# Kernel tuning notes

Measured on AMD Instinct MI355X. Metric: run time of the kernel, lower is better.

## Reference

```python
import jax, jax.numpy as jnp
import numpy as np

B, N, E, H = 2, 2048, 1024, 16
D = E // H  # head dim = 64


def layer_norm(x, gamma, beta, eps=1e-5):
    m = jnp.mean(x, axis=-1, keepdims=True)
    v = jnp.mean(jnp.square(x - m), axis=-1, keepdims=True)
    return (x - m) * jax.lax.rsqrt(v + eps) * gamma + beta


def setup_inputs() -> dict:
    key = jax.random.key(0)
    ks = jax.random.split(key, 9)
    w_scale = 1.0 / np.sqrt(E)
    Q = jax.random.normal(ks[0], (B, N, E), jnp.float32)
    K = jax.random.normal(ks[1], (B, N, E), jnp.float32)
    V = jax.random.normal(ks[2], (B, N, E), jnp.float32)
    # causal mask: True = masked (matches torch masked_fill_ semantics)
    mask = jnp.broadcast_to(jnp.triu(jnp.ones((N, N), bool), k=1)[None, None], (B, 1, N, N))
    Wq = jax.random.normal(ks[3], (E, E), jnp.float32) * w_scale
    Wk = jax.random.normal(ks[4], (E, E), jnp.float32) * w_scale
    Wv = jax.random.normal(ks[5], (E, E), jnp.float32) * w_scale
    bq = jax.random.normal(ks[6], (E,), jnp.float32) * 0.02
    bk = jax.random.normal(ks[7], (E,), jnp.float32) * 0.02
    bv = jax.random.normal(ks[8], (E,), jnp.float32) * 0.02
    gamma = jnp.ones((E,), jnp.float32)
    beta = jnp.zeros((E,), jnp.float32)
    return dict(Q=Q, K=K, V=V, mask=mask, Wq=Wq, bq=bq, Wk=Wk, bk=bk,
                Wv=Wv, bv=bv, gamma=gamma, beta=beta)


def reference(Q, K, V, mask, Wq, bq, Wk, bk, Wv, bv, gamma, beta):
    resid = Q  # cloned_Q residual
    # pre-norm (same LayerNorm applied to all three streams)
    q = layer_norm(Q, gamma, beta) @ Wq + bq  # [B,N,E]
    k = layer_norm(K, gamma, beta) @ Wk + bk
    v = layer_norm(V, gamma, beta) @ Wv + bv
    # split heads -> [B,H,N,D]
    q = q.reshape(B, N, H, D).transpose(0, 2, 1, 3)
    k = k.reshape(B, N, H, D).transpose(0, 2, 1, 3)
    v = v.reshape(B, N, H, D).transpose(0, 2, 1, 3)
    # scores [B,H,N,N], scaled by sqrt(head_dim)
    s = jnp.einsum('bhnd,bhmd->bhnm', q, k) * (D ** -0.5)
    s = jnp.where(mask, -jnp.inf, s)
    p = jax.nn.softmax(s, axis=-1)
    o = jnp.einsum('bhnm,bhmd->bhnd', p, v)
    o = o.transpose(0, 2, 1, 3).reshape(B, N, E)
    return o + resid
```

## Files before the change

### kernel.cpp

```cpp
#include <hip/hip_runtime.h>
#include <hip/hip_bf16.h>

#define B_ 2
#define N_ 2048
#define E_ 1024
#define H_ 16
#define D_ 64
#define M_TOT (B_*N_)

typedef __attribute__((ext_vector_type(8))) short bf16x8;
typedef __attribute__((ext_vector_type(4))) float f32x4;

__device__ __forceinline__ unsigned short f2bf(float f) {
    unsigned int u = __float_as_uint(f);
    u += 0x7fff + ((u >> 16) & 1);
    return (unsigned short)(u >> 16);
}

__device__ __forceinline__ void gload16(const void* g, void* l) {
    __builtin_amdgcn_global_load_lds(
        (const __attribute__((address_space(1))) unsigned int*)g,
        (__attribute__((address_space(3))) unsigned int*)l, 16, 0, 0);
}

__global__ __launch_bounds__(256) void ln_kernel(
    const float* __restrict__ Q, const float* __restrict__ K,
    const float* __restrict__ V, const float* __restrict__ gamma,
    const float* __restrict__ beta, unsigned short* __restrict__ Xn)
{
    const int row = blockIdx.x;
    const int s   = blockIdx.y;
    const float* X = (s == 0) ? Q : (s == 1) ? K : V;
    const int tid = threadIdx.x;
    const float4 x = ((const float4*)(X + (size_t)row * E_))[tid];
    float sum = x.x + x.y + x.z + x.w;
    float sq  = x.x*x.x + x.y*x.y + x.z*x.z + x.w*x.w;
    #pragma unroll
    for (int off = 32; off > 0; off >>= 1) {
        sum += __shfl_down(sum, off);
        sq  += __shfl_down(sq,  off);
    }
    __shared__ float red[8];
    const int wid = tid >> 6;
    if ((tid & 63) == 0) { red[wid] = sum; red[4 + wid] = sq; }
    __syncthreads();
    if (tid == 0) {
        float s0 = red[0] + red[1] + red[2] + red[3];
        float q0 = red[4] + red[5] + red[6] + red[7];
        red[0] = s0 * (1.0f / E_);
        red[4] = q0 * (1.0f / E_);
    }
    __syncthreads();
    const float mean = red[0];
    const float var  = red[4] - mean * mean;
    const float inv  = rsqrtf(var + 1e-5f);
    const float4 g = ((const float4*)gamma)[tid];
    const float4 b = ((const float4*)beta)[tid];
    ushort4 o;
    o.x = f2bf((x.x - mean) * inv * g.x + b.x);
    o.y = f2bf((x.y - mean) * inv * g.y + b.y);
    o.z = f2bf((x.z - mean) * inv * g.z + b.z);
    o.w = f2bf((x.w - mean) * inv * g.w + b.w);
    const int bo = 8 * tid;
    const int bs = (bo & ~127) | ((bo & 127) ^ ((row & 7) << 4));
    char* rowp = (char*)(Xn + (size_t)s * M_TOT * E_ + (size_t)row * E_);
    *(ushort4*)(rowp + bs) = o;
}

__global__ __launch_bounds__(256) void wt_kernel(
    const float* __restrict__ Wq, const float* __restrict__ Wk,
    const float* __restrict__ Wv, unsigned short* __restrict__ Wt)
{
    const int s = blockIdx.z;
    const float* W = (s == 0) ? Wq : (s == 1) ? Wk : Wv;
    __shared__ float tile[32][33];
    const int tx = threadIdx.x, ty = threadIdx.y;
    const int n0 = blockIdx.x * 32, k0 = blockIdx.y * 32;
    #pragma unroll
    for (int i = 0; i < 4; i++)
        tile[ty + 8*i][tx] = W[(size_t)(k0 + ty + 8*i) * E_ + n0 + tx];
    __syncthreads();
    unsigned short* dst = Wt + (size_t)s * E_ * E_;
    #pragma unroll
    for (int i = 0; i < 4; i++) {
        const int n = n0 + ty + 8*i;
        const int bo = 2 * (k0 + tx);
        const int bs = (bo & ~127) | ((bo & 127) ^ ((n & 7) << 4));
        *(unsigned short*)((char*)(dst + (size_t)n * E_) + bs) =
            f2bf(tile[tx][ty + 8*i]);
    }
}

__global__ __launch_bounds__(256, 3) void gemm_kernel(
    const unsigned short* __restrict__ Xn, const unsigned short* __restrict__ Wt,
    const float* __restrict__ bq, const float* __restrict__ bk,
    const float* __restrict__ bv, unsigned short* __restrict__ QKVh)
{
    const int bid = blockIdx.x;
    const int wk  = (bid & 7) * 96 + (bid >> 3);
    const int s   = wk >> 8;
    const int rem = wk & 255;
    const int m0  = (rem >> 3) * 128;
    const int n0  = (rem & 7) * 128;
    const float* bias = (s == 0) ? bq : (s == 1) ? bk : bv;
    const unsigned short* A  = Xn + (size_t)s * M_TOT * E_;
    const unsigned short* Bw = Wt + (size_t)s * E_ * E_;
    unsigned short* out = QKVh + (size_t)s * M_TOT * E_;
    const int tid = threadIdx.x;
    const int lane = tid & 63;
    const int w = tid >> 6;
    const int l15 = lane & 15, lhi = lane >> 4;

    __shared__ unsigned short Al[2][128][64];

    const int srow = lane >> 3;
    const int scol = (lane & 7) * 8;
    const int rx = (l15 & 7) << 4;

    const char* bbase = (const char*)Bw + (size_t)(n0 + w*32 + l15) * (E_ * 2);

    f32x4 acc[8][2];
    #pragma unroll
    for (int m = 0; m < 8; m++)
        #pragma unroll
        for (int n = 0; n < 2; n++)
            acc[m][n] = (f32x4){0.f, 0.f, 0.f, 0.f};

    #define STAGEA(b_, kt_) do {                                             \
        const int k0_ = (kt_) * 64;                                          \
        _Pragma("unroll")                                                    \
        for (int ii = 0; ii < 4; ii++) {                                     \
            const int r_ = w*32 + ii*8;                                      \
            gload16(A + (size_t)(m0 + r_ + srow) * E_ + k0_ + scol,          \
                    &Al[b_][r_][0]);                                         \
        }                                                                    \
    } while (0)

    STAGEA(0, 0);
    for (int kt = 0; kt < 16; kt++) {
        const int buf = kt & 1;
        bf16x8 bfr[2][2];
        #pragma unroll
        for (int ks = 0; ks < 2; ks++)
            #pragma unroll
            for (int n = 0; n < 2; n++)
                bfr[ks][n] = *(const bf16x8*)(bbase + (size_t)n * 16 * (E_ * 2)
                               + kt*128 + ((ks*64 + lhi*16) ^ rx));
        __syncthreads();
        if (kt + 1 < 16) STAGEA(buf ^ 1, kt + 1);
        const char* ab = (const char*)Al[buf];
        #pragma unroll
        for (int ks = 0; ks < 2; ks++) {
            #pragma unroll
            for (int m = 0; m < 8; m++) {
                bf16x8 af = *(const bf16x8*)(ab
                        + (m*16 + l15)*128 + ((ks*64 + lhi*16) ^ rx));
                #pragma unroll
                for (int n = 0; n < 2; n++)
                    acc[m][n] = __builtin_amdgcn_mfma_f32_16x16x32_bf16(
                        af, bfr[ks][n], acc[m][n], 0, 0, 0);
            }
        }
    }
    #undef STAGEA

    const float scale = (s == 0) ? 0.18033688011112042f : 1.0f;
    #pragma unroll
    for (int n = 0; n < 2; n++) {
        const int gn = n0 + w*32 + n*16 + l15;
        const float bv_ = bias[gn];
        const int h = gn >> 6, d = gn & 63;
        #pragma unroll
        for (int m = 0; m < 8; m++) {
            const int gmBase = m0 + m*16 + lhi*4;
            if (s == 2) {
                const int bb2 = gmBase >> 11, nseq = gmBase & 2047;
                ushort4 pk;
                pk.x = f2bf(acc[m][n][0] + bv_);
                pk.y = f2bf(acc[m][n][1] + bv_);
                pk.z = f2bf(acc[m][n][2] + bv_);
                pk.w = f2bf(acc[m][n][3] + bv_);
                *(ushort4*)(out + ((size_t)(bb2*H_ + h) * D_ + d) * N_ + nseq)
                    = pk;
            } else {
                #pragma unroll
                for (int j = 0; j < 4; j++) {
                    const int gm = gmBase + j;
                    const int bb2 = gm >> 11, nseq = gm & 2047;
                    out[((size_t)(bb2*H_ + h) * N_ + nseq) * D_ + d] =
                        f2bf((acc[m][n][j] + bv_) * scale);
                }
            }
        }
    }
}

__global__ __launch_bounds__(512, 4) void attn_kernel(
    const unsigned short* __restrict__ QKVh, const float* __restrict__ Qin,
    float* __restrict__ out)
{
    const int bid  = blockIdx.x;
    const int slot = bid >> 5;
    const int bh   = bid & 31;
    const int g    = 31 - slot;
    const int q0   = g * 64;
    const int S    = (g + 2) >> 1;
    const int tid = threadIdx.x;
    const int lane = tid & 63;
    const int w = tid >> 6;
    const int h = w >> 2;
    const int rg = w & 3;
    const int l15 = lane & 15, lhi = lane >> 4;
    const size_t headOff = (size_t)bh * N_ * D_;
    const unsigned short* qh = QKVh + headOff;
    const unsigned short* kh = QKVh + (size_t)M_TOT * E_ + headOff;
    const unsigned short* vh = QKVh + (size_t)2 * M_TOT * E_ + headOff;

    __shared__ unsigned short Kt[2][64*64];
    __shared__ unsigned short Vt[2][64*64];
    __shared__ unsigned short Pl[8][16*64];
    __shared__ float Ml[4][16];

    const int sr  = (tid >> 3) & 63;
    const int sce = (tid & 7) * 8;
    const int wofs = sr * 128 + (((tid & 7) * 16) ^ ((sr & 7) << 4));
    const int rxor = (l15 & 7) << 4;

    const int bb = bh >> 4, hh = bh & 15;
    const int wlo = q0 + rg * 16;

    {
        uint4 ka  = *(const uint4*)(kh + (size_t)sr * D_ + sce);
        uint4 kb2 = *(const uint4*)(kh + (size_t)(64 + sr) * D_ + sce);
        uint4 va  = *(const uint4*)(vh + (size_t)sr * N_ + sce);
        uint4 vb2 = *(const uint4*)(vh + (size_t)sr * N_ + 64 + sce);
        *(uint4*)((char*)Kt[0] + wofs) = ka;
        *(uint4*)((char*)Kt[1] + wofs) = kb2;
        *(uint4*)((char*)Vt[0] + wofs) = va;
        *(uint4*)((char*)Vt[1] + wofs) = vb2;
    }

    bf16x8 qf[2];
    #pragma unroll
    for (int ks = 0; ks < 2; ks++)
        qf[ks] = *(const bf16x8*)(qh + (size_t)(wlo + l15) * D_
                                      + ks*32 + lhi*8);

    const f32x4 fz = {0.f, 0.f, 0.f, 0.f};
    f32x4 o[4], ol;
    #pragma unroll
    for (int n = 0; n < 4; n++) o[n] = fz;
    ol = fz;
    bf16x8 ones;
    #pragma unroll
    for (int i = 0; i < 8; i++) ones[i] = (short)0x3F80;

    #pragma unroll 1
    for (int s = 0; s < S; s++) {
        __syncthreads();
        uint4 nka, nkb, nva, nvb;
        const bool pre = (s + 1 < S);
        if (pre) {
            const int kvn = (s + 1) * 128;
            nka = *(const uint4*)(kh + (size_t)(kvn + sr) * D_ + sce);
            nkb = *(const uint4*)(kh + (size_t)(kvn + 64 + sr) * D_ + sce);
            nva = *(const uint4*)(vh + (size_t)sr * N_ + kvn + sce);
            nvb = *(const uint4*)(vh + (size_t)sr * N_ + kvn + 64 + sce);
        }
        const int t = 2*s + h;
        if (t <= g) {
            const int kv0 = t * 64;
            const char* kbb = (const char*)Kt[t & 1];
            const char* vbb = (const char*)Vt[t & 1];
            f32x4 sfr[4];
            #pragma unroll
            for (int n = 0; n < 4; n++) sfr[n] = fz;
            #pragma unroll
            for (int ks = 0; ks < 2; ks++) {
                bf16x8 kb[4];
                #pragma unroll
                for (int n = 0; n < 4; n++)
                    kb[n] = *(const bf16x8*)(kbb + (n*16 + l15)*128
                                                 + ((ks*64 + lhi*16) ^ rxor));
                __builtin_amdgcn_s_setprio(1);
                #pragma unroll
                for (int n = 0; n < 4; n++)
                    sfr[n] = __builtin_amdgcn_mfma_f32_16x16x32_bf16(
                        kb[n], qf[ks], sfr[n], 0, 0, 0);
                __builtin_amdgcn_s_setprio(0);
            }
            const int qr = wlo + l15;
            if (t == g) {
                #pragma unroll
                for (int n = 0; n < 4; n++)
                    #pragma unroll
                    for (int j = 0; j < 4; j++) {
                        int kvc = kv0 + n*16 + lhi*4 + j;
                        sfr[n][j] = (kvc > qr) ? -1e30f : sfr[n][j];
                    }
            }
            char* pw = (char*)Pl[w];
            #pragma unroll
            for (int n = 0; n < 4; n++) {
                unsigned int u0 = __float_as_uint(exp2f(sfr[n][0])) + 0x8000u;
                unsigned int u1 = __float_as_uint(exp2f(sfr[n][1])) + 0x8000u;
                unsigned int u2 = __float_as_uint(exp2f(sfr[n][2])) + 0x8000u;
                unsigned int u3 = __float_as_uint(exp2f(sfr[n][3])) + 0x8000u;
                uint2 pk;
                pk.x = __builtin_amdgcn_perm(u1, u0, 0x07060302u);
                pk.y = __builtin_amdgcn_perm(u3, u2, 0x07060302u);
                *(uint2*)(pw + l15*128 + ((n*32 + lhi*8) ^ rxor)) = pk;
            }
            #pragma unroll
            for (int ks = 0; ks < 2; ks++) {
                bf16x8 pb = *(const bf16x8*)(pw + l15*128
                                             + ((ks*64 + lhi*16) ^ rxor));
                bf16x8 vbr[4];
                #pragma unroll
                for (int n = 0; n < 4; n++)
                    vbr[n] = *(const bf16x8*)(vbb + (n*16 + l15)*128
                                                  + ((ks*64 + lhi*16) ^ rxor));
                __builtin_amdgcn_s_setprio(1);
                #pragma unroll
                for (int n = 0; n < 4; n++)
                    o[n] = __builtin_amdgcn_mfma_f32_16x16x32_bf16(
                        vbr[n], pb, o[n], 0, 0, 0);
                ol = __builtin_amdgcn_mfma_f32_16x16x32_bf16(
                    ones, pb, ol, 0, 0, 0);
                __builtin_amdgcn_s_setprio(0);
            }
        }
        __syncthreads();
        if (pre) {
            *(uint4*)((char*)Kt[0] + wofs) = nka;
            *(uint4*)((char*)Kt[1] + wofs) = nkb;
            *(uint4*)((char*)Vt[0] + wofs) = nva;
            *(uint4*)((char*)Vt[1] + wofs) = nvb;
        }
    }

    const float l_i = ol[0];
    __syncthreads();
    if (h == 1) {
        char* ob = (char*)Pl + rg * 4096;
        #pragma unroll
        for (int n = 0; n < 4; n++)
            *(f32x4*)(ob + l15*256 + ((n*64 + lhi*16) ^ rxor)) = o[n];
        if (lhi == 0) Ml[rg][l15] = l_i;
    }
    __syncthreads();
    if (h == 0) {
        const float linv = 1.0f / (l_i + Ml[rg][l15]);
        const char* ob = (const char*)Pl + rg * 4096;
        const int qr = wlo + l15;
        #pragma unroll
        for (int n = 0; n < 4; n++) {
            f32x4 o1 = *(const f32x4*)(ob + l15*256 + ((n*64 + lhi*16) ^ rxor));
            const int d0 = n*16 + lhi*4;
            size_t idx = ((size_t)(bb * N_ + qr)) * E_ + hh * D_ + d0;
            float4 r = *(const float4*)(Qin + idx);
            float4 ov;
            ov.x = (o[n][0] + o1[0]) * linv + r.x;
            ov.y = (o[n][1] + o1[1]) * linv + r.y;
            ov.z = (o[n][2] + o1[2]) * linv + r.z;
            ov.w = (o[n][3] + o1[3]) * linv + r.w;
            *(float4*)(out + idx) = ov;
        }
    }
}

extern "C" void kernel_launch(void* const* d_in, const int* in_sizes, int n_in,
                              void* d_out, int out_size, void* d_ws, size_t ws_size,
                              hipStream_t stream) {
    const float* Q     = (const float*)d_in[0];
    const float* K     = (const float*)d_in[1];
    const float* V     = (const float*)d_in[2];
    const float* Wq    = (const float*)d_in[4];
    const float* bq    = (const float*)d_in[5];
    const float* Wk    = (const float*)d_in[6];
    const float* bk    = (const float*)d_in[7];
    const float* Wv    = (const float*)d_in[8];
    const float* bv    = (const float*)d_in[9];
    const float* gamma = (const float*)d_in[10];
    const float* beta  = (const float*)d_in[11];
    float* out = (float*)d_out;

    char* ws = (char*)d_ws;
    unsigned short* Xn   = (unsigned short*)ws;
    unsigned short* Wt   = (unsigned short*)(ws + 25165824);
    unsigned short* QKVh = (unsigned short*)(ws + 31457280);

    ln_kernel  <<<dim3(4096, 3),   256,        0, stream>>>(Q, K, V, gamma, beta, Xn);
    wt_kernel  <<<dim3(32, 32, 3), dim3(32,8), 0, stream>>>(Wq, Wk, Wv, Wt);
    gemm_kernel<<<dim3(768),       256,        0, stream>>>(Xn, Wt, bq, bk, bv, QKVh);
    attn_kernel<<<dim3(1024),      512,        0, stream>>>(QKVh, Q, out);
}
```

Baseline: 93.40 us.

## Double attention query tile per block to 128 rows, halving grid

Each attention block now handles 128 query rows instead of 64, with each wave computing two 16-row query sub-tiles. This reuses every K/V tile loaded into shared memory and every K/V fragment read from LDS across twice as many queries, which cuts global and LDS traffic per unit of work. The grid halves to 512 blocks and launch bounds drop to 2 blocks per CU to make room for the doubled register accumulators and larger P buffers. In exchange there is less parallelism and occupancy, coarser causal load balance, and more register pressure.

```diff
diff --git a/kernel.cpp b/kernel.cpp
--- a/kernel.cpp
+++ b/kernel.cpp
@@ -195,31 +195,32 @@
     }
 }
 
-__global__ __launch_bounds__(512, 4) void attn_kernel(
+__global__ __launch_bounds__(512, 2) void attn_kernel(
     const unsigned short* __restrict__ QKVh, const float* __restrict__ Qin,
     float* __restrict__ out)
 {
     const int bid  = blockIdx.x;
     const int slot = bid >> 5;
     const int bh   = bid & 31;
-    const int g    = 31 - slot;
-    const int q0   = g * 64;
-    const int S    = (g + 2) >> 1;
+    const int gg   = 15 - slot;
+    const int q0   = gg * 128;
+    const int S    = gg + 1;
     const int tid = threadIdx.x;
     const int lane = tid & 63;
     const int w = tid >> 6;
     const int h = w >> 2;
     const int rg = w & 3;
     const int l15 = lane & 15, lhi = lane >> 4;
+    const int tdg = 2*gg + (rg >> 1);
     const size_t headOff = (size_t)bh * N_ * D_;
-    const unsigned short* qh = QKVh + headOff;
+    const unsigned short* qp = QKVh + headOff;
     const unsigned short* kh = QKVh + (size_t)M_TOT * E_ + headOff;
     const unsigned short* vh = QKVh + (size_t)2 * M_TOT * E_ + headOff;
 
     __shared__ unsigned short Kt[2][64*64];
     __shared__ unsigned short Vt[2][64*64];
-    __shared__ unsigned short Pl[8][16*64];
-    __shared__ float Ml[4][16];
+    __shared__ unsigned short Pl[8][32*64];
+    __shared__ float Ml[4][32];
 
     const int sr  = (tid >> 3) & 63;
     const int sce = (tid & 7) * 8;
@@ -227,7 +228,7 @@
     const int rxor = (l15 & 7) << 4;
 
     const int bb = bh >> 4, hh = bh & 15;
-    const int wlo = q0 + rg * 16;
+    const int wlo = q0 + rg * 32;
 
     {
         uint4 ka  = *(const uint4*)(kh + (size_t)sr * D_ + sce);
@@ -240,20 +241,29 @@
         *(uint4*)((char*)Vt[1] + wofs) = vb2;
     }
 
-    bf16x8 qf[2];
-    #pragma unroll
-    for (int ks = 0; ks < 2; ks++)
-        qf[ks] = *(const bf16x8*)(qh + (size_t)(wlo + l15) * D_
-                                      + ks*32 + lhi*8);
+    bf16x8 qf[2][2];
+    #pragma unroll
+    for (int qh = 0; qh < 2; qh++)
+        #pragma unroll
+        for (int ks = 0; ks < 2; ks++)
+            qf[qh][ks] = *(const bf16x8*)(qp
+                + (size_t)(wlo + qh*16 + l15) * D_ + ks*32 + lhi*8);
 
     const f32x4 fz = {0.f, 0.f, 0.f, 0.f};
-    f32x4 o[4], ol;
-    #pragma unroll
-    for (int n = 0; n < 4; n++) o[n] = fz;
-    ol = fz;
+    f32x4 o[2][4], ol[2];
+    #pragma unroll
+    for (int qh = 0; qh < 2; qh++) {
+        ol[qh] = fz;
+        #pragma unroll
+        for (int n = 0; n < 4; n++) o[qh][n] = fz;
+    }
     bf16x8 ones;
     #pragma unroll
     for (int i = 0; i < 8; i++) ones[i] = (short)0x3F80;
+
+    char* pw = (char*)Pl[w];
+    const char* kbb = (const char*)Kt[h];
+    const char* vbb = (const char*)Vt[h];
 
     #pragma unroll 1
     for (int s = 0; s < S; s++) {
@@ -268,13 +278,12 @@
             nvb = *(const uint4*)(vh + (size_t)sr * N_ + kvn + 64 + sce);
         }
         const int t = 2*s + h;
-        if (t <= g) {
-            const int kv0 = t * 64;
-            const char* kbb = (const char*)Kt[t & 1];
-            const char* vbb = (const char*)Vt[t & 1];
-            f32x4 sfr[4];
-            #pragma unroll
-            for (int n = 0; n < 4; n++) sfr[n] = fz;
+        if (t <= tdg) {
+            f32x4 sf[2][4];
+            #pragma unroll
+            for (int qh = 0; qh < 2; qh++)
+                #pragma unroll
+                for (int n = 0; n < 4; n++) sf[qh][n] = fz;
             #pragma unroll
             for (int ks = 0; ks < 2; ks++) {
                 bf16x8 kb[4];
@@ -284,37 +293,48 @@
                                                  + ((ks*64 + lhi*16) ^ rxor));
                 __builtin_amdgcn_s_setprio(1);
                 #pragma unroll
-                for (int n = 0; n < 4; n++)
-                    sfr[n] = __builtin_amdgcn_mfma_f32_16x16x32_bf16(
-                        kb[n], qf[ks], sfr[n], 0, 0, 0);
+                for (int qh = 0; qh < 2; qh++)
+                    #pragma unroll
+                    for (int n = 0; n < 4; n++)
+                        sf[qh][n] = __builtin_amdgcn_mfma_f32_16x16x32_bf16(
+                            kb[n], qf[qh][ks], sf[qh][n], 0, 0, 0);
                 __builtin_amdgcn_s_setprio(0);
             }
-            const int qr = wlo + l15;
-            if (t == g) {
-                #pragma unroll
-                for (int n = 0; n < 4; n++)
+            if (t == tdg) {
+                #pragma unroll
+                for (int qh = 0; qh < 2; qh++) {
+                    const int qr = wlo + qh*16 + l15;
                     #pragma unroll
-                    for (int j = 0; j < 4; j++) {
-                        int kvc = kv0 + n*16 + lhi*4 + j;
-                        sfr[n][j] = (kvc > qr) ? -1e30f : sfr[n][j];
-                    }
-            }
-            char* pw = (char*)Pl[w];
-            #pragma unroll
-            for (int n = 0; n < 4; n++) {
-                unsigned int u0 = __float_as_uint(exp2f(sfr[n][0])) + 0x8000u;
-                unsigned int u1 = __float_as_uint(exp2f(sfr[n][1])) + 0x8000u;
-                unsigned int u2 = __float_as_uint(exp2f(sfr[n][2])) + 0x8000u;
-                unsigned int u3 = __float_as_uint(exp2f(sfr[n][3])) + 0x8000u;
-                uint2 pk;
-                pk.x = __builtin_amdgcn_perm(u1, u0, 0x07060302u);
-                pk.y = __builtin_amdgcn_perm(u3, u2, 0x07060302u);
-                *(uint2*)(pw + l15*128 + ((n*32 + lhi*8) ^ rxor)) = pk;
+                    for (int n = 0; n < 4; n++)
+                        #pragma unroll
+                        for (int j = 0; j < 4; j++) {
+                            int kvc = t*64 + n*16 + lhi*4 + j;
+                            sf[qh][n][j] = (kvc > qr) ? -1e30f : sf[qh][n][j];
+                        }
+                }
+            }
+            #pragma unroll
+            for (int qh = 0; qh < 2; qh++) {
+                const int prow = (qh*16 + l15) * 128;
+                #pragma unroll
+                for (int n = 0; n < 4; n++) {
+                    unsigned int u0 = __float_as_uint(exp2f(sf[qh][n][0])) + 0x8000u;
+                    unsigned int u1 = __float_as_uint(exp2f(sf[qh][n][1])) + 0x8000u;
+                    unsigned int u2 = __float_as_uint(exp2f(sf[qh][n][2])) + 0x8000u;
+                    unsigned int u3 = __float_as_uint(exp2f(sf[qh][n][3])) + 0x8000u;
+                    uint2 pk;
+                    pk.x = __builtin_amdgcn_perm(u1, u0, 0x07060302u);
+                    pk.y = __builtin_amdgcn_perm(u3, u2, 0x07060302u);
+                    *(uint2*)(pw + prow + ((n*32 + lhi*8) ^ rxor)) = pk;
+                }
             }
             #pragma unroll
             for (int ks = 0; ks < 2; ks++) {
-                bf16x8 pb = *(const bf16x8*)(pw + l15*128
-                                             + ((ks*64 + lhi*16) ^ rxor));
+                bf16x8 pb[2];
+                #pragma unroll
+                for (int qh = 0; qh < 2; qh++)
+                    pb[qh] = *(const bf16x8*)(pw + (qh*16 + l15)*128
+                                                 + ((ks*64 + lhi*16) ^ rxor));
                 bf16x8 vbr[4];
                 #pragma unroll
                 for (int n = 0; n < 4; n++)
@@ -322,11 +342,16 @@
                                                   + ((ks*64 + lhi*16) ^ rxor));
                 __builtin_amdgcn_s_setprio(1);
                 #pragma unroll
-                for (int n = 0; n < 4; n++)
-                    o[n] = __builtin_amdgcn_mfma_f32_16x16x32_bf16(
-                        vbr[n], pb, o[n], 0, 0, 0);
-                ol = __builtin_amdgcn_mfma_f32_16x16x32_bf16(
-                    ones, pb, ol, 0, 0, 0);
+                for (int n = 0; n < 4; n++) {
+                    o[0][n] = __builtin_amdgcn_mfma_f32_16x16x32_bf16(
+                        vbr[n], pb[0], o[0][n], 0, 0, 0);
+                    o[1][n] = __builtin_amdgcn_mfma_f32_16x16x32_bf16(
+                        vbr[n], pb[1], o[1][n], 0, 0, 0);
+                }
+                ol[0] = __builtin_amdgcn_mfma_f32_16x16x32_bf16(
+                    ones, pb[0], ol[0], 0, 0, 0);
+                ol[1] = __builtin_amdgcn_mfma_f32_16x16x32_bf16(
+                    ones, pb[1], ol[1], 0, 0, 0);
                 __builtin_amdgcn_s_setprio(0);
             }
         }
@@ -339,32 +364,38 @@
         }
     }
 
-    const float l_i = ol[0];
     __syncthreads();
     if (h == 1) {
-        char* ob = (char*)Pl + rg * 4096;
-        #pragma unroll
-        for (int n = 0; n < 4; n++)
-            *(f32x4*)(ob + l15*256 + ((n*64 + lhi*16) ^ rxor)) = o[n];
-        if (lhi == 0) Ml[rg][l15] = l_i;
+        char* ob = (char*)Pl + rg * 8192;
+        #pragma unroll
+        for (int qh = 0; qh < 2; qh++)
+            #pragma unroll
+            for (int n = 0; n < 4; n++)
+                *(f32x4*)(ob + (qh*16 + l15)*256 + ((n*64 + lhi*16) ^ rxor))
+                    = o[qh][n];
+        if (lhi == 0) { Ml[rg][l15] = ol[0][0]; Ml[rg][16 + l15] = ol[1][0]; }
     }
     __syncthreads();
     if (h == 0) {
-        const float linv = 1.0f / (l_i + Ml[rg][l15]);
-        const char* ob = (const char*)Pl + rg * 4096;
-        const int qr = wlo + l15;
-        #pragma unroll
-        for (int n = 0; n < 4; n++) {
-            f32x4 o1 = *(const f32x4*)(ob + l15*256 + ((n*64 + lhi*16) ^ rxor));
-            const int d0 = n*16 + lhi*4;
-            size_t idx = ((size_t)(bb * N_ + qr)) * E_ + hh * D_ + d0;
-            float4 r = *(const float4*)(Qin + idx);
-            float4 ov;
-            ov.x = (o[n][0] + o1[0]) * linv + r.x;
-            ov.y = (o[n][1] + o1[1]) * linv + r.y;
-            ov.z = (o[n][2] + o1[2]) * linv + r.z;
-            ov.w = (o[n][3] + o1[3]) * linv + r.w;
-            *(float4*)(out + idx) = ov;
+        const char* ob = (const char*)Pl + rg * 8192;
+        #pragma unroll
+        for (int qh = 0; qh < 2; qh++) {
+            const float linv = 1.0f / (ol[qh][0] + Ml[rg][qh*16 + l15]);
+            const int qr = wlo + qh*16 + l15;
+            #pragma unroll
+            for (int n = 0; n < 4; n++) {
+                f32x4 o1 = *(const f32x4*)(ob + (qh*16 + l15)*256
+                                              + ((n*64 + lhi*16) ^ rxor));
+                const int d0 = n*16 + lhi*4;
+                size_t idx = ((size_t)(bb * N_ + qr)) * E_ + hh * D_ + d0;
+                float4 r = *(const float4*)(Qin + idx);
+                float4 ov;
+                ov.x = (o[qh][n][0] + o1[0]) * linv + r.x;
+                ov.y = (o[qh][n][1] + o1[1]) * linv + r.y;
+                ov.z = (o[qh][n][2] + o1[2]) * linv + r.z;
+                ov.w = (o[qh][n][3] + o1[3]) * linv + r.w;
+                *(float4*)(out + idx) = ov;
+            }
         }
     }
 }
@@ -393,5 +424,5 @@
     ln_kernel  <<<dim3(4096, 3),   256,        0, stream>>>(Q, K, V, gamma, beta, Xn);
     wt_kernel  <<<dim3(32, 32, 3), dim3(32,8), 0, stream>>>(Wq, Wk, Wv, Wt);
     gemm_kernel<<<dim3(768),       256,        0, stream>>>(Xn, Wt, bq, bk, bv, QKVh);
-    attn_kernel<<<dim3(1024),      512,        0, stream>>>(QKVh, Q, out);
-}
+    attn_kernel<<<dim3(512),       512,        0, stream>>>(QKVh, Q, out);
+}
```

Result: slower. 95.80 us (+2.6%).
